# Optimization experiments

Hardware: AMD Instinct MI355X
Metric: run time of the kernel (lower is better)

Reference implementation:

```python
import jax, jax.numpy as jnp
import numpy as np

T_MAX = 0.5
LN_EPS = 1e-5
B, N, D = 256, 16384, 512
NNZ = N * 33  # ~ (2*top_k+1) nonzeros per row of the sparse Laplacian
DF = 4 * D
DT = 32  # time-embedding hidden size


def _layernorm(x, g, b):
    mu = jnp.mean(x, axis=-1, keepdims=True)
    var = jnp.mean((x - mu) ** 2, axis=-1, keepdims=True)
    return (x - mu) * jax.lax.rsqrt(var + LN_EPS) * g + b


def setup_inputs() -> dict:
    key = jax.random.key(0)
    ks = jax.random.split(key, 16)

    def lin_w(k, fan_out, fan_in):
        return jax.random.normal(k, (fan_out, fan_in), jnp.float32) * (1.0 / np.sqrt(fan_in))

    inp = {}
    inp["x0"] = jax.random.uniform(ks[0], (B, N), jnp.float32)
    inp["t"] = jax.random.uniform(ks[1], (B,), jnp.float32)
    inp["L_vals"] = jax.random.normal(ks[2], (NNZ,), jnp.float32) * 0.1
    inp["W_in"] = lin_w(ks[3], D, N)
    inp["b_in"] = jnp.zeros((D,), jnp.float32)
    inp["W_out"] = lin_w(ks[4], N, D)
    inp["b_out"] = jnp.zeros((N,), jnp.float32)
    inp["W_qkv"] = lin_w(ks[5], 3 * D, D)
    inp["b_qkv"] = jnp.zeros((3 * D,), jnp.float32)
    inp["W_o"] = lin_w(ks[6], D, D)
    inp["b_o"] = jnp.zeros((D,), jnp.float32)
    inp["g1"] = jnp.ones((D,), jnp.float32)
    inp["be1"] = jnp.zeros((D,), jnp.float32)
    inp["g2"] = jnp.ones((D,), jnp.float32)
    inp["be2"] = jnp.zeros((D,), jnp.float32)
    inp["W_f1"] = lin_w(ks[7], DF, D)
    inp["b_f1"] = jnp.zeros((DF,), jnp.float32)
    inp["W_f2"] = lin_w(ks[8], D, DF)
    inp["b_f2"] = jnp.zeros((D,), jnp.float32)
    inp["W_t1"] = lin_w(ks[9], DT, 1)
    inp["b_t1"] = jnp.zeros((DT,), jnp.float32)
    inp["W_t2"] = lin_w(ks[10], D, DT)
    inp["b_t2"] = jnp.zeros((D,), jnp.float32)
    inp["L_rows"] = jax.random.randint(ks[11], (NNZ,), 0, N, jnp.int32)
    inp["L_cols"] = jax.random.randint(ks[12], (NNZ,), 0, N, jnp.int32)
    return inp


def reference(x0, t, L_vals, W_in, b_in, W_out, b_out, W_qkv, b_qkv, W_o, b_o,
              g1, be1, g2, be2, W_f1, b_f1, W_f2, b_f2, W_t1, b_t1, W_t2, b_t2,
              L_rows, L_cols):
    n_items = x0.shape[1]
    d_model = W_in.shape[0]
    t_cont = t * T_MAX  # per-sample diffusion time (explicit input, not RNG)

    # Batched sparse Laplacian diffusion (replaces the per-row torch.sparse.mm loop):
    # (L @ x.T)[i, b] = sum_e L_vals[e] * x0[b, L_cols[e]] aggregated to row L_rows[e]
    contrib = x0[:, L_cols] * L_vals                                  # (B, NNZ)
    Lx = jax.ops.segment_sum(contrib.T, L_rows, num_segments=n_items)  # (N, B)
    x_t = x0 - t_cont[:, None] * Lx.T                                  # (B, N)

    # Denoiser (eval mode: dropout off)
    h = x_t @ W_in.T + b_in                                            # (B, D)
    t_norm = t_cont / T_MAX
    te = jax.nn.silu(t_norm[:, None] @ W_t1.T + b_t1) @ W_t2.T + b_t2  # (B, D)
    h = h + te

    # MultiheadAttention on a length-1 sequence: softmax over one key is exactly 1,
    # so attn_out = out_proj(V) with V = h @ W_v.T + b_v.
    qkv = h @ W_qkv.T + b_qkv                                          # (B, 3D)
    v = qkv[:, 2 * d_model:]
    attn_out = v @ W_o.T + b_o

    h = _layernorm(h + attn_out, g1, be1)
    ff = jax.nn.gelu(h @ W_f1.T + b_f1, approximate=False) @ W_f2.T + b_f2
    h = _layernorm(h + ff, g2, be2)

    pred = h @ W_out.T + b_out                                         # (B, N)
    return jnp.mean((pred - x0) ** 2)
```

## Files before the change

kernel.cpp:

```cpp
#include <hip/hip_runtime.h>
#include <math.h>

#define Bb   256
#define Nn   16384
#define Dd   512
#define NNZn 540672
#define DFf  2048
#define SLOT 128

#define CVT_BLKS 2560
#define TR_BLKS  1024
#define BK_BLKS  2112

typedef __bf16 bf16;
typedef __bf16 bf16x4 __attribute__((ext_vector_type(4)));
typedef __bf16 bf16x8 __attribute__((ext_vector_type(8)));
typedef float  f32x4  __attribute__((ext_vector_type(4)));

__device__ __forceinline__ void gload16(const void* g, void* l) {
  __builtin_amdgcn_global_load_lds(
      (const __attribute__((address_space(1))) unsigned int*)g,
      (__attribute__((address_space(3))) unsigned int*)l, 16, 0, 0);
}

__global__ __launch_bounds__(256) void k_prep(
    const float* __restrict__ w_v, const float* __restrict__ w_o,
    const float* __restrict__ w_f1, const float* __restrict__ w_f2,
    bf16* __restrict__ o_v, bf16* __restrict__ o_o,
    bf16* __restrict__ o_f1, bf16* __restrict__ o_f2,
    const float* __restrict__ x0, bf16* __restrict__ x0T,
    const int* __restrict__ rows, const int* __restrict__ cols,
    const float* __restrict__ vals,
    int* __restrict__ counts, int2* __restrict__ ents) {
  __shared__ float tile[64][65];
  int blk = blockIdx.x;
  if (blk < CVT_BLKS) {
    int v = blk * 256 + threadIdx.x;
    const float* s; bf16* d; int base;
    if (v < 131072) {
      if (v < 65536) { s = w_v;  d = o_v;  base = 0; }
      else           { s = w_o;  d = o_o;  base = 65536; }
    } else {
      if (v < 393216) { s = w_f1; d = o_f1; base = 131072; }
      else            { s = w_f2; d = o_f2; base = 393216; }
    }
    int idx = (v - base) * 4;
    float4 x = *(const float4*)(s + idx);
    bf16x4 o;
    o[0] = (bf16)x.x; o[1] = (bf16)x.y; o[2] = (bf16)x.z; o[3] = (bf16)x.w;
    *(bf16x4*)(d + idx) = o;
  } else if (blk < CVT_BLKS + TR_BLKS) {
    int bx = blk - CVT_BLKS;
    int n0 = (bx & 255) * 64, b0 = (bx >> 8) * 64;
    int tx = threadIdx.x & 63, ty = threadIdx.x >> 6;
#pragma unroll
    for (int i = 0; i < 16; i++) {
      int bl = ty * 16 + i;
      tile[bl][tx] = x0[(size_t)(b0 + bl) * Nn + n0 + tx];
    }
    __syncthreads();
#pragma unroll
    for (int i = 0; i < 16; i++) {
      int nl = ty * 16 + i;
      x0T[(size_t)(n0 + nl) * Bb + b0 + tx] = (bf16)tile[tx][nl];
    }
  } else {
    int i = (blk - CVT_BLKS - TR_BLKS) * 256 + threadIdx.x;
    int r = rows[i];
    int p = atomicAdd(&counts[r], 1);
    if (p < SLOT)
      ents[(size_t)r * SLOT + p] = make_int2(cols[i], __float_as_int(vals[i]));
  }
}

__global__ __launch_bounds__(256) void k_lx(const bf16x4* __restrict__ x0T4,
                                            const int* __restrict__ counts,
                                            const int2* __restrict__ ents,
                                            bf16x4* __restrict__ Lx4) {
  int w = threadIdx.x >> 6, lane = threadIdx.x & 63;
  int r = blockIdx.x * 4 + w;
  __shared__ int2 esm[4][64];
  int cnt = counts[r];
  const int2* ep = ents + (size_t)r * SLOT;
  float a0 = 0.f, a1 = 0.f, a2 = 0.f, a3 = 0.f;
  float b0 = 0.f, b1 = 0.f, b2 = 0.f, b3 = 0.f;
  for (int base = 0; base < cnt; base += 64) {
    int m = cnt - base; if (m > 64) m = 64;
    if (lane < m) esm[w][lane] = ep[base + lane];
    int i = 0;
    for (; i + 1 < m; i += 2) {
      int2 e0 = esm[w][i], e1 = esm[w][i + 1];
      bf16x4 xv0 = x0T4[(size_t)e0.x * 64 + lane];
      bf16x4 xv1 = x0T4[(size_t)e1.x * 64 + lane];
      float v0 = __int_as_float(e0.y), v1 = __int_as_float(e1.y);
      a0 += v0 * (float)xv0[0]; a1 += v0 * (float)xv0[1];
      a2 += v0 * (float)xv0[2]; a3 += v0 * (float)xv0[3];
      b0 += v1 * (float)xv1[0]; b1 += v1 * (float)xv1[1];
      b2 += v1 * (float)xv1[2]; b3 += v1 * (float)xv1[3];
    }
    if (i < m) {
      int2 e0 = esm[w][i];
      bf16x4 xv0 = x0T4[(size_t)e0.x * 64 + lane];
      float v0 = __int_as_float(e0.y);
      a0 += v0 * (float)xv0[0]; a1 += v0 * (float)xv0[1];
      a2 += v0 * (float)xv0[2]; a3 += v0 * (float)xv0[3];
    }
  }
  bf16x4 o;
  o[0] = (bf16)(a0 + b0); o[1] = (bf16)(a1 + b1);
  o[2] = (bf16)(a2 + b2); o[3] = (bf16)(a3 + b3);
  Lx4[(size_t)r * 64 + lane] = o;
}

__global__ __launch_bounds__(256) void k_combine(const float* __restrict__ x0,
                                                 const bf16* __restrict__ Lx,
                                                 const float* __restrict__ t,
                                                 bf16* __restrict__ xt) {
  __shared__ float lxs[64][65];
  int n0 = blockIdx.x * 64, b0 = blockIdx.y * 64;
  int tx = threadIdx.x & 63, ty = threadIdx.x >> 6;
#pragma unroll
  for (int i = 0; i < 16; i++) {
    int nl = ty * 16 + i;
    lxs[nl][tx] = (float)Lx[(size_t)(n0 + nl) * Bb + b0 + tx];
  }
  __syncthreads();
#pragma unroll
  for (int i = 0; i < 16; i++) {
    int bl = ty * 16 + i;
    int b  = b0 + bl;
    float tc = t[b] * 0.5f;
    float v = x0[(size_t)b * Nn + n0 + tx] - tc * lxs[tx][bl];
    xt[(size_t)b * Nn + n0 + tx] = (bf16)v;
  }
}

template <int BM, int BN, int MODE, int ACT = 0, int BF32 = 0>
__global__ __launch_bounds__(256) void gemm_tn(
    const bf16* __restrict__ A, const void* __restrict__ Bmv,
    float* __restrict__ C, int N, int K, int kLen, int MN,
    const float* __restrict__ bias, const float* __restrict__ x0,
    float* __restrict__ lossOut) {
  constexpr int WM = BM / 2, WN = BN / 2, FM = WM / 16, FN = WN / 16;
  constexpr int PA = (BM * 64) / 4096, PB = (BN * 64) / 4096;
  __shared__ __align__(16) bf16 As[BM * 32];
  __shared__ __align__(16) bf16 Bs[BN * 32];
  const int tid = threadIdx.x;
  const int lane = tid & 63, w = tid >> 6;
  const int wm = w >> 1, wn = w & 1;
  const int mBase = blockIdx.x * BM, nBase = blockIdx.y * BN;
  const int k0 = blockIdx.z * kLen;

  f32x4 acc[FM][FN];
#pragma unroll
  for (int i = 0; i < FM; i++)
#pragma unroll
    for (int j = 0; j < FN; j++) acc[i][j] = {0.f, 0.f, 0.f, 0.f};

  for (int kk = 0; kk < kLen; kk += 32) {
    const int k = k0 + kk;
    __syncthreads();
#pragma unroll
    for (int p = 0; p < PA; p++) {
      int u = p * 256 + tid;
      gload16(A + (size_t)(mBase + (u >> 2)) * K + k + (u & 3) * 8,
              (char*)As + p * 4096 + w * 1024);
    }
    if constexpr (BF32) {
      const float* Bf = (const float*)Bmv;
#pragma unroll
      for (int p = 0; p < BN * 32 / 1024; p++) {
        int u = p * 256 + tid;
        int row = u >> 3, sub = u & 7;
        float4 x = *(const float4*)(Bf + (size_t)(nBase + row) * K + k + sub * 4);
        bf16x4 o;
        o[0] = (bf16)x.x; o[1] = (bf16)x.y; o[2] = (bf16)x.z; o[3] = (bf16)x.w;
        *(bf16x4*)(Bs + row * 32 + sub * 4) = o;
      }
    } else {
      const bf16* Bm = (const bf16*)Bmv;
#pragma unroll
      for (int p = 0; p < PB; p++) {
        int u = p * 256 + tid;
        gload16(Bm + (size_t)(nBase + (u >> 2)) * K + k + (u & 3) * 8,
                (char*)Bs + p * 4096 + w * 1024);
      }
    }
    __syncthreads();
    bf16x8 af[FM], bfr[FN];
#pragma unroll
    for (int i = 0; i < FM; i++)
      af[i] = *(const bf16x8*)(As + (wm * WM + i * 16 + (lane & 15)) * 32 + (lane >> 4) * 8);
#pragma unroll
    for (int j = 0; j < FN; j++)
      bfr[j] = *(const bf16x8*)(Bs + (wn * WN + j * 16 + (lane & 15)) * 32 + (lane >> 4) * 8);
#pragma unroll
    for (int i = 0; i < FM; i++)
#pragma unroll
      for (int j = 0; j < FN; j++)
        acc[i][j] = __builtin_amdgcn_mfma_f32_16x16x32_bf16(af[i], bfr[j], acc[i][j], 0, 0, 0);
  }

  if constexpr (MODE == 0) {
    float* Cz = C + (size_t)blockIdx.z * MN;
#pragma unroll
    for (int i = 0; i < FM; i++)
#pragma unroll
      for (int j = 0; j < FN; j++) {
        int n  = nBase + wn * WN + j * 16 + (lane & 15);
        int mB = mBase + wm * WM + i * 16 + ((lane >> 4) << 2);
#pragma unroll
        for (int r = 0; r < 4; r++)
          Cz[(size_t)(mB + r) * N + n] = acc[i][j][r];
      }
  } else if constexpr (MODE == 1) {
    bf16* Cb = (bf16*)C;
#pragma unroll
    for (int i = 0; i < FM; i++)
#pragma unroll
      for (int j = 0; j < FN; j++) {
        int n  = nBase + wn * WN + j * 16 + (lane & 15);
        float bo = bias[n];
        int mB = mBase + wm * WM + i * 16 + ((lane >> 4) << 2);
#pragma unroll
        for (int r = 0; r < 4; r++) {
          float x = acc[i][j][r] + bo;
          if constexpr (ACT == 1)
            x = 0.5f * x * (1.f + erff(x * 0.70710678118654752f));
          Cb[(size_t)(mB + r) * N + n] = (bf16)x;
        }
      }
  } else {
    float lsum = 0.f;
#pragma unroll
    for (int i = 0; i < FM; i++)
#pragma unroll
      for (int j = 0; j < FN; j++) {
        int n  = nBase + wn * WN + j * 16 + (lane & 15);
        float bo = bias[n];
        int mB = mBase + wm * WM + i * 16 + ((lane >> 4) << 2);
#pragma unroll
        for (int r = 0; r < 4; r++) {
          float d = acc[i][j][r] + bo - x0[(size_t)(mB + r) * N + n];
          lsum += d * d;
        }
      }
    for (int off = 32; off > 0; off >>= 1) lsum += __shfl_down(lsum, off, 64);
    if (lane == 0) atomicAdd(lossOut, lsum);
  }
}

__global__ __launch_bounds__(512) void k_epi_h(const float* __restrict__ P,
                                               const float* __restrict__ t,
                                               const float* __restrict__ W_t1,
                                               const float* __restrict__ b_t1,
                                               const float* __restrict__ W_t2,
                                               const float* __restrict__ b_t2,
                                               const float* __restrict__ b_in,
                                               float* __restrict__ h_f32,
                                               bf16* __restrict__ h_b) {
  int b = blockIdx.x, d = threadIdx.x;
  __shared__ float s[32];
  if (d < 32) {
    float z = t[b] * W_t1[d] + b_t1[d];
    s[d] = z / (1.f + expf(-z));
  }
  __syncthreads();
  int i = b * Dd + d;
  float v = b_in[d] + b_t2[d];
#pragma unroll
  for (int sp = 0; sp < 32; sp++) v += P[sp * (Bb * Dd) + i];
#pragma unroll
  for (int j = 0; j < 32; j++) v += s[j] * W_t2[d * 32 + j];
  h_f32[i] = v;
  h_b[i] = (bf16)v;
}

template <int NS>
__global__ __launch_bounds__(512) void k_ln(const float* __restrict__ base,
                                            const float* __restrict__ add,
                                            const float* __restrict__ bias,
                                            const float* __restrict__ g,
                                            const float* __restrict__ be,
                                            float* __restrict__ out_f32,
                                            bf16* __restrict__ out_b) {
  int b = blockIdx.x, d = threadIdx.x;
  __shared__ float red[16];
  int i = b * Dd + d;
  float x = base[i] + bias[d];
#pragma unroll
  for (int sp = 0; sp < NS; sp++) x += add[sp * (Bb * Dd) + i];
  int w = d >> 6, lane = d & 63;
  float s = x;
  for (int off = 32; off > 0; off >>= 1) s += __shfl_down(s, off, 64);
  if (lane == 0) red[w] = s;
  __syncthreads();
  if (d == 0) {
    float tot = 0.f;
    for (int q = 0; q < 8; q++) tot += red[q];
    red[8] = tot * (1.f / 512.f);
  }
  __syncthreads();
  float mu = red[8];
  float c = x - mu;
  float s2 = c * c;
  for (int off = 32; off > 0; off >>= 1) s2 += __shfl_down(s2, off, 64);
  if (lane == 0) red[w] = s2;
  __syncthreads();
  if (d == 0) {
    float tot = 0.f;
    for (int q = 0; q < 8; q++) tot += red[q];
    red[8] = tot * (1.f / 512.f);
  }
  __syncthreads();
  float var = red[8];
  float y = c * rsqrtf(var + 1e-5f) * g[d] + be[d];
  if (out_f32) out_f32[i] = y;
  out_b[i] = (bf16)y;
}

__global__ void k_final(const float* __restrict__ loss, float* __restrict__ out) {
  if (threadIdx.x == 0 && blockIdx.x == 0)
    out[0] = loss[0] * (1.f / 4194304.f);
}

extern "C" void kernel_launch(void* const* d_in, const int* in_sizes, int n_in,
                              void* d_out, int out_size, void* d_ws, size_t ws_size,
                              hipStream_t stream) {
  const float* x0    = (const float*)d_in[0];
  const float* t     = (const float*)d_in[1];
  const float* Lv    = (const float*)d_in[2];
  const float* W_in  = (const float*)d_in[3];
  const float* b_in  = (const float*)d_in[4];
  const float* W_out = (const float*)d_in[5];
  const float* b_out = (const float*)d_in[6];
  const float* W_qkv = (const float*)d_in[7];
  const float* b_qkv = (const float*)d_in[8];
  const float* W_o   = (const float*)d_in[9];
  const float* b_o   = (const float*)d_in[10];
  const float* g1    = (const float*)d_in[11];
  const float* be1   = (const float*)d_in[12];
  const float* g2    = (const float*)d_in[13];
  const float* be2   = (const float*)d_in[14];
  const float* W_f1  = (const float*)d_in[15];
  const float* b_f1  = (const float*)d_in[16];
  const float* W_f2  = (const float*)d_in[17];
  const float* b_f2  = (const float*)d_in[18];
  const float* W_t1  = (const float*)d_in[19];
  const float* b_t1  = (const float*)d_in[20];
  const float* W_t2  = (const float*)d_in[21];
  const float* b_t2  = (const float*)d_in[22];
  const int* L_rows  = (const int*)d_in[23];
  const int* L_cols  = (const int*)d_in[24];

  size_t off = 0;
  char* ws = (char*)d_ws;
  auto carve = [&](size_t bytes) -> void* {
    void* p = ws + off;
    off += (bytes + 255) & ~(size_t)255;
    return p;
  };

  bf16* W_v_b    = (bf16*)carve((size_t)Dd * Dd * 2);
  bf16* W_o_b    = (bf16*)carve((size_t)Dd * Dd * 2);
  bf16* W_f1_b   = (bf16*)carve((size_t)DFf * Dd * 2);
  bf16* W_f2_b   = (bf16*)carve((size_t)Dd * DFf * 2);
  bf16* x0T_b    = (bf16*)carve((size_t)Nn * Bb * 2);
  bf16* Lx_b     = (bf16*)carve((size_t)Nn * Bb * 2);
  bf16* xt_b     = (bf16*)carve((size_t)Bb * Nn * 2);
  float* p_h     = (float*)carve((size_t)32 * Bb * Dd * 4);
  float* p_at    = (float*)carve((size_t)Bb * Dd * 4);
  float* p_f2    = (float*)carve((size_t)4 * Bb * Dd * 4);
  float* h_f32   = (float*)carve((size_t)Bb * Dd * 4);
  bf16* h_b      = (bf16*)carve((size_t)Bb * Dd * 2);
  bf16* v_b      = (bf16*)carve((size_t)Bb * Dd * 2);
  float* hln_f32 = (float*)carve((size_t)Bb * Dd * 4);
  bf16* hln_b    = (bf16*)carve((size_t)Bb * Dd * 2);
  bf16* f1_b     = (bf16*)carve((size_t)Bb * DFf * 2);
  bf16* h2_b     = (bf16*)carve((size_t)Bb * Dd * 2);
  int* counts    = (int*)carve((size_t)Nn * 4);
  float* lossw   = (float*)carve(256);
  int2* ents     = (int2*)carve((size_t)Nn * SLOT * 8);
  (void)in_sizes; (void)n_in; (void)out_size; (void)ws_size; (void)Lv;

  hipMemsetAsync(counts, 0, (size_t)Nn * 4 + 256, stream);

  k_prep<<<CVT_BLKS + TR_BLKS + BK_BLKS, 256, 0, stream>>>(
      W_qkv + (size_t)2 * Dd * Dd, W_o, W_f1, W_f2,
      W_v_b, W_o_b, W_f1_b, W_f2_b,
      x0, x0T_b, L_rows, L_cols, Lv, counts, ents);

  k_lx<<<Nn / 4, 256, 0, stream>>>((const bf16x4*)x0T_b, counts, ents,
                                   (bf16x4*)Lx_b);
  k_combine<<<dim3(256, 4), 256, 0, stream>>>(x0, Lx_b, t, xt_b);

  gemm_tn<128, 128, 0, 0, 1><<<dim3(2, 4, 32), 256, 0, stream>>>(
      xt_b, W_in, p_h, Dd, Nn, 512, Bb * Dd, nullptr, nullptr, nullptr);
  k_epi_h<<<Bb, 512, 0, stream>>>(p_h, t, W_t1, b_t1, W_t2, b_t2, b_in, h_f32, h_b);

  gemm_tn<64, 64, 1><<<dim3(4, 8, 1), 256, 0, stream>>>(
      h_b, W_v_b, (float*)v_b, Dd, Dd, 512, 0, b_qkv + 2 * Dd, nullptr, nullptr);

  gemm_tn<64, 64, 0><<<dim3(4, 8, 1), 256, 0, stream>>>(
      v_b, W_o_b, p_at, Dd, Dd, 512, 0, nullptr, nullptr, nullptr);
  k_ln<1><<<Bb, 512, 0, stream>>>(h_f32, p_at, b_o, g1, be1, hln_f32, hln_b);

  gemm_tn<64, 64, 1, 1><<<dim3(4, 32, 1), 256, 0, stream>>>(
      hln_b, W_f1_b, (float*)f1_b, DFf, Dd, 512, 0, b_f1, nullptr, nullptr);

  gemm_tn<64, 64, 0><<<dim3(4, 8, 4), 256, 0, stream>>>(
      f1_b, W_f2_b, p_f2, Dd, DFf, 512, Bb * Dd, nullptr, nullptr, nullptr);
  k_ln<4><<<Bb, 512, 0, stream>>>(hln_f32, p_f2, b_f2, g2, be2, nullptr, h2_b);

  gemm_tn<128, 128, 2, 0, 1><<<dim3(2, 128, 1), 256, 0, stream>>>(
      h2_b, W_out, nullptr, Nn, Dd, 512, 0, b_out, x0, lossw);
  k_final<<<1, 64, 0, stream>>>(lossw, (float*)d_out);
}
```

Measured before the change: 329.6 us.

## Fold V and out-proj weights, halve split-K, fuse loss finalize, unroll Lx gather

```diff
diff --git a/kernel.cpp b/kernel.cpp
--- a/kernel.cpp
+++ b/kernel.cpp
@@ -8,9 +8,17 @@
 #define DFf  2048
 #define SLOT 128
 
-#define CVT_BLKS 2560
-#define TR_BLKS  1024
-#define BK_BLKS  2112
+#define BK_BLKS 528
+#define TR_BLKS 1024
+#define CVT_BLKS 2048
+#define MG_BLKS 64
+#define BV_BLKS 2
+#define BK0 0
+#define TR0 (BK0 + BK_BLKS)
+#define CVT0 (TR0 + TR_BLKS)
+#define MG0 (CVT0 + CVT_BLKS)
+#define BV0 (MG0 + MG_BLKS)
+#define PREP_BLKS (BV0 + BV_BLKS)
 
 typedef __bf16 bf16;
 typedef __bf16 bf16x4 __attribute__((ext_vector_type(4)));
@@ -26,50 +34,123 @@
 __global__ __launch_bounds__(256) void k_prep(
     const float* __restrict__ w_v, const float* __restrict__ w_o,
     const float* __restrict__ w_f1, const float* __restrict__ w_f2,
-    bf16* __restrict__ o_v, bf16* __restrict__ o_o,
     bf16* __restrict__ o_f1, bf16* __restrict__ o_f2,
+    bf16* __restrict__ w_ov,
+    const float* __restrict__ b_o, const float* __restrict__ b_v,
+    float* __restrict__ bsum,
     const float* __restrict__ x0, bf16* __restrict__ x0T,
     const int* __restrict__ rows, const int* __restrict__ cols,
     const float* __restrict__ vals,
     int* __restrict__ counts, int2* __restrict__ ents) {
   __shared__ float tile[64][65];
-  int blk = blockIdx.x;
-  if (blk < CVT_BLKS) {
-    int v = blk * 256 + threadIdx.x;
+  __shared__ __align__(16) bf16 As[64 * 32];
+  __shared__ __align__(16) bf16 Bs[64 * 32];
+  const int blk = blockIdx.x, tid = threadIdx.x;
+
+  if (blk < TR0) {
+    int i0 = blk * 1024 + tid;
+    int r[4], c[4]; float v[4];
+#pragma unroll
+    for (int q = 0; q < 4; q++) {
+      int i = i0 + q * 256;
+      r[q] = rows[i]; c[q] = cols[i]; v[q] = vals[i];
+    }
+    int p[4];
+#pragma unroll
+    for (int q = 0; q < 4; q++) p[q] = atomicAdd(&counts[r[q]], 1);
+#pragma unroll
+    for (int q = 0; q < 4; q++)
+      if (p[q] < SLOT)
+        ents[(size_t)r[q] * SLOT + p[q]] = make_int2(c[q], __float_as_int(v[q]));
+  } else if (blk < CVT0) {
+    int bx = blk - TR0;
+    int n0 = (bx & 255) * 64, b0 = (bx >> 8) * 64;
+    int tx = tid & 63, ty = tid >> 6;
+#pragma unroll
+    for (int i = 0; i < 16; i++) {
+      int bl = ty * 16 + i;
+      tile[bl][tx] = x0[(size_t)(b0 + bl) * Nn + n0 + tx];
+    }
+    __syncthreads();
+#pragma unroll
+    for (int i = 0; i < 16; i++) {
+      int nl = ty * 16 + i;
+      x0T[(size_t)(n0 + nl) * Bb + b0 + tx] = (bf16)tile[tx][nl];
+    }
+  } else if (blk < MG0) {
+    int v4 = (blk - CVT0) * 256 + tid;
     const float* s; bf16* d; int base;
-    if (v < 131072) {
-      if (v < 65536) { s = w_v;  d = o_v;  base = 0; }
-      else           { s = w_o;  d = o_o;  base = 65536; }
-    } else {
-      if (v < 393216) { s = w_f1; d = o_f1; base = 131072; }
-      else            { s = w_f2; d = o_f2; base = 393216; }
-    }
-    int idx = (v - base) * 4;
+    if (v4 < 262144) { s = w_f1; d = o_f1; base = 0; }
+    else             { s = w_f2; d = o_f2; base = 262144; }
+    int idx = (v4 - base) * 4;
     float4 x = *(const float4*)(s + idx);
     bf16x4 o;
     o[0] = (bf16)x.x; o[1] = (bf16)x.y; o[2] = (bf16)x.z; o[3] = (bf16)x.w;
     *(bf16x4*)(d + idx) = o;
-  } else if (blk < CVT_BLKS + TR_BLKS) {
-    int bx = blk - CVT_BLKS;
-    int n0 = (bx & 255) * 64, b0 = (bx >> 8) * 64;
-    int tx = threadIdx.x & 63, ty = threadIdx.x >> 6;
-#pragma unroll
-    for (int i = 0; i < 16; i++) {
-      int bl = ty * 16 + i;
-      tile[bl][tx] = x0[(size_t)(b0 + bl) * Nn + n0 + tx];
-    }
-    __syncthreads();
-#pragma unroll
-    for (int i = 0; i < 16; i++) {
-      int nl = ty * 16 + i;
-      x0T[(size_t)(n0 + nl) * Bb + b0 + tx] = (bf16)tile[tx][nl];
-    }
+  } else if (blk < BV0) {
+    int mg = blk - MG0;
+    int m0 = (mg >> 3) * 64, n0 = (mg & 7) * 64;
+    const int lane = tid & 63, w = tid >> 6;
+    const int wm = w >> 1, wn = w & 1;
+    f32x4 acc[2][2];
+#pragma unroll
+    for (int i = 0; i < 2; i++)
+#pragma unroll
+      for (int j = 0; j < 2; j++) acc[i][j] = {0.f, 0.f, 0.f, 0.f};
+    for (int e0 = 0; e0 < Dd; e0 += 32) {
+      __syncthreads();
+#pragma unroll
+      for (int p = 0; p < 2; p++) {
+        int u = p * 256 + tid;
+        int row = u >> 3, sub = u & 7;
+        float4 x = *(const float4*)(w_o + (size_t)(m0 + row) * Dd + e0 + sub * 4);
+        bf16x4 o;
+        o[0] = (bf16)x.x; o[1] = (bf16)x.y; o[2] = (bf16)x.z; o[3] = (bf16)x.w;
+        *(bf16x4*)(As + row * 32 + sub * 4) = o;
+      }
+#pragma unroll
+      for (int p = 0; p < 2; p++) {
+        int u = p * 256 + tid;
+        int el = u >> 4, jq = u & 15;
+        float4 x = *(const float4*)(w_v + (size_t)(e0 + el) * Dd + n0 + jq * 4);
+        Bs[(jq * 4 + 0) * 32 + el] = (bf16)x.x;
+        Bs[(jq * 4 + 1) * 32 + el] = (bf16)x.y;
+        Bs[(jq * 4 + 2) * 32 + el] = (bf16)x.z;
+        Bs[(jq * 4 + 3) * 32 + el] = (bf16)x.w;
+      }
+      __syncthreads();
+      bf16x8 af[2], bfr[2];
+#pragma unroll
+      for (int i = 0; i < 2; i++)
+        af[i] = *(const bf16x8*)(As + (wm * 32 + i * 16 + (lane & 15)) * 32 + (lane >> 4) * 8);
+#pragma unroll
+      for (int j = 0; j < 2; j++)
+        bfr[j] = *(const bf16x8*)(Bs + (wn * 32 + j * 16 + (lane & 15)) * 32 + (lane >> 4) * 8);
+#pragma unroll
+      for (int i = 0; i < 2; i++)
+#pragma unroll
+        for (int j = 0; j < 2; j++)
+          acc[i][j] = __builtin_amdgcn_mfma_f32_16x16x32_bf16(af[i], bfr[j], acc[i][j], 0, 0, 0);
+    }
+#pragma unroll
+    for (int i = 0; i < 2; i++)
+#pragma unroll
+      for (int j = 0; j < 2; j++) {
+        int jj = n0 + wn * 32 + j * 16 + (lane & 15);
+        int dB = m0 + wm * 32 + i * 16 + ((lane >> 4) << 2);
+#pragma unroll
+        for (int r = 0; r < 4; r++)
+          w_ov[(size_t)(dB + r) * Dd + jj] = (bf16)acc[i][j][r];
+      }
   } else {
-    int i = (blk - CVT_BLKS - TR_BLKS) * 256 + threadIdx.x;
-    int r = rows[i];
-    int p = atomicAdd(&counts[r], 1);
-    if (p < SLOT)
-      ents[(size_t)r * SLOT + p] = make_int2(cols[i], __float_as_int(vals[i]));
+    int d = (blk - BV0) * 256 + tid;
+    float s = b_o[d];
+    for (int e = 0; e < Dd; e += 4) {
+      float4 wo = *(const float4*)(w_o + (size_t)d * Dd + e);
+      float4 bv = *(const float4*)(b_v + e);
+      s += wo.x * bv.x + wo.y * bv.y + wo.z * bv.z + wo.w * bv.w;
+    }
+    bsum[d] = s;
   }
 }
 
@@ -82,33 +163,39 @@
   __shared__ int2 esm[4][64];
   int cnt = counts[r];
   const int2* ep = ents + (size_t)r * SLOT;
-  float a0 = 0.f, a1 = 0.f, a2 = 0.f, a3 = 0.f;
-  float b0 = 0.f, b1 = 0.f, b2 = 0.f, b3 = 0.f;
+  f32x4 a = {0.f, 0.f, 0.f, 0.f}, b = {0.f, 0.f, 0.f, 0.f};
+  f32x4 c = {0.f, 0.f, 0.f, 0.f}, d = {0.f, 0.f, 0.f, 0.f};
   for (int base = 0; base < cnt; base += 64) {
     int m = cnt - base; if (m > 64) m = 64;
     if (lane < m) esm[w][lane] = ep[base + lane];
     int i = 0;
-    for (; i + 1 < m; i += 2) {
-      int2 e0 = esm[w][i], e1 = esm[w][i + 1];
-      bf16x4 xv0 = x0T4[(size_t)e0.x * 64 + lane];
-      bf16x4 xv1 = x0T4[(size_t)e1.x * 64 + lane];
+    for (; i + 3 < m; i += 4) {
+      int2 e0 = esm[w][i], e1 = esm[w][i + 1], e2 = esm[w][i + 2], e3 = esm[w][i + 3];
+      bf16x4 x0v = x0T4[(size_t)e0.x * 64 + lane];
+      bf16x4 x1v = x0T4[(size_t)e1.x * 64 + lane];
+      bf16x4 x2v = x0T4[(size_t)e2.x * 64 + lane];
+      bf16x4 x3v = x0T4[(size_t)e3.x * 64 + lane];
       float v0 = __int_as_float(e0.y), v1 = __int_as_float(e1.y);
-      a0 += v0 * (float)xv0[0]; a1 += v0 * (float)xv0[1];
-      a2 += v0 * (float)xv0[2]; a3 += v0 * (float)xv0[3];
-      b0 += v1 * (float)xv1[0]; b1 += v1 * (float)xv1[1];
-      b2 += v1 * (float)xv1[2]; b3 += v1 * (float)xv1[3];
-    }
-    if (i < m) {
+      float v2 = __int_as_float(e2.y), v3 = __int_as_float(e3.y);
+#pragma unroll
+      for (int q = 0; q < 4; q++) {
+        a[q] += v0 * (float)x0v[q];
+        b[q] += v1 * (float)x1v[q];
+        c[q] += v2 * (float)x2v[q];
+        d[q] += v3 * (float)x3v[q];
+      }
+    }
+    for (; i < m; i++) {
       int2 e0 = esm[w][i];
-      bf16x4 xv0 = x0T4[(size_t)e0.x * 64 + lane];
+      bf16x4 x0v = x0T4[(size_t)e0.x * 64 + lane];
       float v0 = __int_as_float(e0.y);
-      a0 += v0 * (float)xv0[0]; a1 += v0 * (float)xv0[1];
-      a2 += v0 * (float)xv0[2]; a3 += v0 * (float)xv0[3];
+#pragma unroll
+      for (int q = 0; q < 4; q++) a[q] += v0 * (float)x0v[q];
     }
   }
   bf16x4 o;
-  o[0] = (bf16)(a0 + b0); o[1] = (bf16)(a1 + b1);
-  o[2] = (bf16)(a2 + b2); o[3] = (bf16)(a3 + b3);
+#pragma unroll
+  for (int q = 0; q < 4; q++) o[q] = (bf16)(a[q] + b[q] + c[q] + d[q]);
   Lx4[(size_t)r * 64 + lane] = o;
 }
 
@@ -140,7 +227,7 @@
     const bf16* __restrict__ A, const void* __restrict__ Bmv,
     float* __restrict__ C, int N, int K, int kLen, int MN,
     const float* __restrict__ bias, const float* __restrict__ x0,
-    float* __restrict__ lossOut) {
+    float* __restrict__ lossOut, float* __restrict__ finalOut, int nWaves) {
   constexpr int WM = BM / 2, WN = BN / 2, FM = WM / 16, FN = WN / 16;
   constexpr int PA = (BM * 64) / 4096, PB = (BN * 64) / 4096;
   __shared__ __align__(16) bf16 As[BM * 32];
@@ -246,10 +333,19 @@
         }
       }
     for (int off = 32; off > 0; off >>= 1) lsum += __shfl_down(lsum, off, 64);
-    if (lane == 0) atomicAdd(lossOut, lsum);
-  }
-}
-
+    if (lane == 0) {
+      atomicAdd(lossOut, lsum);
+      __threadfence();
+      unsigned prev = atomicAdd((unsigned*)(lossOut + 1), 1u);
+      if ((int)prev == nWaves - 1) {
+        float tot = atomicAdd(lossOut, 0.f);
+        finalOut[0] = tot * (1.f / 4194304.f);
+      }
+    }
+  }
+}
+
+template <int NS>
 __global__ __launch_bounds__(512) void k_epi_h(const float* __restrict__ P,
                                                const float* __restrict__ t,
                                                const float* __restrict__ W_t1,
@@ -269,7 +365,7 @@
   int i = b * Dd + d;
   float v = b_in[d] + b_t2[d];
 #pragma unroll
-  for (int sp = 0; sp < 32; sp++) v += P[sp * (Bb * Dd) + i];
+  for (int sp = 0; sp < NS; sp++) v += P[sp * (Bb * Dd) + i];
 #pragma unroll
   for (int j = 0; j < 32; j++) v += s[j] * W_t2[d * 32 + j];
   h_f32[i] = v;
@@ -317,11 +413,6 @@
   float y = c * rsqrtf(var + 1e-5f) * g[d] + be[d];
   if (out_f32) out_f32[i] = y;
   out_b[i] = (bf16)y;
-}
-
-__global__ void k_final(const float* __restrict__ loss, float* __restrict__ out) {
-  if (threadIdx.x == 0 && blockIdx.x == 0)
-    out[0] = loss[0] * (1.f / 4194304.f);
 }
 
 extern "C" void kernel_launch(void* const* d_in, const int* in_sizes, int n_in,
@@ -361,19 +452,18 @@
     return p;
   };
 
-  bf16* W_v_b    = (bf16*)carve((size_t)Dd * Dd * 2);
-  bf16* W_o_b    = (bf16*)carve((size_t)Dd * Dd * 2);
+  bf16* W_ov_b   = (bf16*)carve((size_t)Dd * Dd * 2);
   bf16* W_f1_b   = (bf16*)carve((size_t)DFf * Dd * 2);
   bf16* W_f2_b   = (bf16*)carve((size_t)Dd * DFf * 2);
+  float* bsum    = (float*)carve((size_t)Dd * 4);
   bf16* x0T_b    = (bf16*)carve((size_t)Nn * Bb * 2);
   bf16* Lx_b     = (bf16*)carve((size_t)Nn * Bb * 2);
   bf16* xt_b     = (bf16*)carve((size_t)Bb * Nn * 2);
-  float* p_h     = (float*)carve((size_t)32 * Bb * Dd * 4);
+  float* p_h     = (float*)carve((size_t)16 * Bb * Dd * 4);
   float* p_at    = (float*)carve((size_t)Bb * Dd * 4);
   float* p_f2    = (float*)carve((size_t)4 * Bb * Dd * 4);
   float* h_f32   = (float*)carve((size_t)Bb * Dd * 4);
   bf16* h_b      = (bf16*)carve((size_t)Bb * Dd * 2);
-  bf16* v_b      = (bf16*)carve((size_t)Bb * Dd * 2);
   float* hln_f32 = (float*)carve((size_t)Bb * Dd * 4);
   bf16* hln_b    = (bf16*)carve((size_t)Bb * Dd * 2);
   bf16* f1_b     = (bf16*)carve((size_t)Bb * DFf * 2);
@@ -385,34 +475,32 @@
 
   hipMemsetAsync(counts, 0, (size_t)Nn * 4 + 256, stream);
 
-  k_prep<<<CVT_BLKS + TR_BLKS + BK_BLKS, 256, 0, stream>>>(
-      W_qkv + (size_t)2 * Dd * Dd, W_o, W_f1, W_f2,
-      W_v_b, W_o_b, W_f1_b, W_f2_b,
+  k_prep<<<PREP_BLKS, 256, 0, stream>>>(
+      W_qkv + (size_t)2 * Dd * Dd, W_o, W_f1, W_f2, W_f1_b, W_f2_b,
+      W_ov_b, b_o, b_qkv + 2 * Dd, bsum,
       x0, x0T_b, L_rows, L_cols, Lv, counts, ents);
 
   k_lx<<<Nn / 4, 256, 0, stream>>>((const bf16x4*)x0T_b, counts, ents,
                                    (bf16x4*)Lx_b);
   k_combine<<<dim3(256, 4), 256, 0, stream>>>(x0, Lx_b, t, xt_b);
 
-  gemm_tn<128, 128, 0, 0, 1><<<dim3(2, 4, 32), 256, 0, stream>>>(
-      xt_b, W_in, p_h, Dd, Nn, 512, Bb * Dd, nullptr, nullptr, nullptr);
-  k_epi_h<<<Bb, 512, 0, stream>>>(p_h, t, W_t1, b_t1, W_t2, b_t2, b_in, h_f32, h_b);
-
-  gemm_tn<64, 64, 1><<<dim3(4, 8, 1), 256, 0, stream>>>(
-      h_b, W_v_b, (float*)v_b, Dd, Dd, 512, 0, b_qkv + 2 * Dd, nullptr, nullptr);
+  gemm_tn<128, 128, 0, 0, 1><<<dim3(2, 4, 16), 256, 0, stream>>>(
+      xt_b, W_in, p_h, Dd, Nn, 1024, Bb * Dd, nullptr, nullptr, nullptr, nullptr, 0);
+  k_epi_h<16><<<Bb, 512, 0, stream>>>(p_h, t, W_t1, b_t1, W_t2, b_t2, b_in,
+                                      h_f32, h_b);
 
   gemm_tn<64, 64, 0><<<dim3(4, 8, 1), 256, 0, stream>>>(
-      v_b, W_o_b, p_at, Dd, Dd, 512, 0, nullptr, nullptr, nullptr);
-  k_ln<1><<<Bb, 512, 0, stream>>>(h_f32, p_at, b_o, g1, be1, hln_f32, hln_b);
+      h_b, W_ov_b, p_at, Dd, Dd, 512, 0, nullptr, nullptr, nullptr, nullptr, 0);
+  k_ln<1><<<Bb, 512, 0, stream>>>(h_f32, p_at, bsum, g1, be1, hln_f32, hln_b);
 
   gemm_tn<64, 64, 1, 1><<<dim3(4, 32, 1), 256, 0, stream>>>(
-      hln_b, W_f1_b, (float*)f1_b, DFf, Dd, 512, 0, b_f1, nullptr, nullptr);
+      hln_b, W_f1_b, (float*)f1_b, DFf, Dd, 512, 0, b_f1, nullptr, nullptr, nullptr, 0);
 
   gemm_tn<64, 64, 0><<<dim3(4, 8, 4), 256, 0, stream>>>(
-      f1_b, W_f2_b, p_f2, Dd, DFf, 512, Bb * Dd, nullptr, nullptr, nullptr);
+      f1_b, W_f2_b, p_f2, Dd, DFf, 512, Bb * Dd, nullptr, nullptr, nullptr, nullptr, 0);
   k_ln<4><<<Bb, 512, 0, stream>>>(hln_f32, p_f2, b_f2, g2, be2, nullptr, h2_b);
 
   gemm_tn<128, 128, 2, 0, 1><<<dim3(2, 128, 1), 256, 0, stream>>>(
-      h2_b, W_out, nullptr, Nn, Dd, 512, 0, b_out, x0, lossw);
-  k_final<<<1, 64, 0, stream>>>(lossw, (float*)d_out);
-}
+      h2_b, W_out, nullptr, Nn, Dd, 512, 0, b_out, x0, lossw,
+      (float*)d_out, 2 * 128 * 4);
+}
```

After: 365.2 us. 1.11x slower.
